# Kernel tuning notes

Hardware: AMD Instinct MI355X
Metric: run time of the kernel (lower is better)

## Reference

```python
import jax, jax.numpy as jnp
import numpy as np

N = 50000      # nodes
DIN = 512      # in_channels == in_gnn_channels == out_channels
H = 2          # num_heads
C = 512        # per-head out_channels of TransConvLayer (== in_channels)
DEMB = 256     # in_embed_features
NE = 800000    # edges (unused by transformer path)
ALPHA = 0.5
LN_EPS = 1e-5


def setup_inputs() -> dict:
    key = jax.random.key(0)
    ks = jax.random.split(key, 24)
    w = lambda k, shape, s=0.02: jax.random.normal(k, shape, jnp.float32) * s
    inp = {}
    inp["x"] = jax.random.normal(ks[0], (N, DIN), jnp.float32)
    inp["gnn_x"] = jax.random.normal(ks[1], (N, DIN), jnp.float32)
    inp["embed_x"] = jax.random.normal(ks[2], (N, DEMB), jnp.float32)
    inp["edge_index"] = jax.random.randint(ks[3], (2, NE), 0, N)
    # trans_conv input fc + layernorm
    inp["fc0_w"] = w(ks[4], (DIN, DIN)); inp["fc0_b"] = jnp.zeros((DIN,), jnp.float32)
    inp["ln0_g"] = jnp.ones((DIN,), jnp.float32); inp["ln0_b"] = jnp.zeros((DIN,), jnp.float32)
    # two TransConvLayers: Wq/Wk/Wv Linear(DIN, C*H) + post layernorm
    for i in range(2):
        base = 5 + i * 7
        inp[f"wq{i}_w"] = w(ks[base + 0], (DIN, C * H)); inp[f"wq{i}_b"] = jnp.zeros((C * H,), jnp.float32)
        inp[f"wk{i}_w"] = w(ks[base + 1], (DIN, C * H)); inp[f"wk{i}_b"] = jnp.zeros((C * H,), jnp.float32)
        inp[f"wv{i}_w"] = w(ks[base + 2], (DIN, C * H)); inp[f"wv{i}_b"] = jnp.zeros((C * H,), jnp.float32)
        inp[f"ln{i+1}_g"] = jnp.ones((DIN,), jnp.float32); inp[f"ln{i+1}_b"] = jnp.zeros((DIN,), jnp.float32)
    # SGFormer output projections: W_r (no bias), fc
    inp["wr_w"] = w(ks[20], (DIN, DIN))
    inp["fc_w"] = w(ks[21], (DIN, DIN)); inp["fc_b"] = jnp.zeros((DIN,), jnp.float32)
    return inp


def _layernorm(h, g, b):
    mu = jnp.mean(h, axis=-1, keepdims=True)
    var = jnp.mean(jnp.square(h - mu), axis=-1, keepdims=True)
    return (h - mu) * jax.lax.rsqrt(var + LN_EPS) * g + b


def _full_attention_conv(qs, ks, vs):
    # qs, ks, vs: [N, H, C]; global (Frobenius) L2 normalization, as in torch.norm(x, p=2)
    qs = qs / jnp.linalg.norm(qs)
    ks = ks / jnp.linalg.norm(ks)
    n = qs.shape[0]
    kvs = jnp.einsum('lhm,lhd->hmd', ks, vs)                   # [H, C, C]
    attn_num = jnp.einsum('nhm,hmd->nhd', qs, kvs) + n * vs    # [N, H, C]
    ks_sum = jnp.sum(ks, axis=0)                               # [H, C]
    norm = jnp.einsum('nhm,hm->nh', qs, ks_sum)[..., None] + n  # [N, H, 1]
    return attn_num / norm


def _trans_layer(h, wq_w, wq_b, wk_w, wk_b, wv_w, wv_b):
    q = (h @ wq_w + wq_b).reshape(-1, H, C)
    k = (h @ wk_w + wk_b).reshape(-1, H, C)
    v = (h @ wv_w + wv_b).reshape(-1, H, C)
    return jnp.mean(_full_attention_conv(q, k, v), axis=1)     # mean over heads -> [N, C]


def reference(x, gnn_x, embed_x, edge_index,
              fc0_w, fc0_b, ln0_g, ln0_b,
              wq0_w, wq0_b, wk0_w, wk0_b, wv0_w, wv0_b, ln1_g, ln1_b,
              wq1_w, wq1_b, wk1_w, wk1_b, wv1_w, wv1_b, ln2_g, ln2_b,
              wr_w, fc_w, fc_b):
    # use_graph=False: x, embed_x, edge_index are dead inputs (torch code computes
    # unused x_atten / scores; output depends only on gnn_x path). Eval mode: dropout off.
    h = jax.nn.relu(_layernorm(gnn_x @ fc0_w + fc0_b, ln0_g, ln0_b))
    layer_params = [
        (wq0_w, wq0_b, wk0_w, wk0_b, wv0_w, wv0_b, ln1_g, ln1_b),
        (wq1_w, wq1_b, wk1_w, wk1_b, wv1_w, wv1_b, ln2_g, ln2_b),
    ]
    for (qw, qb, kw, kb, vw, vb, lg, lb) in layer_params:
        a = _trans_layer(h, qw, qb, kw, kb, vw, vb)
        h = _layernorm(ALPHA * a + (1.0 - ALPHA) * h, lg, lb)
    return (h @ wr_w) @ fc_w + fc_b
```

## Files before the change

### kernel.cpp

```cpp
#include <hip/hip_runtime.h>

#define NN 50000
#define D 512
#define DD (512 * 512)
#define ROWS 64

typedef __attribute__((ext_vector_type(4))) float f32x4;
typedef __attribute__((ext_vector_type(8))) short bf16x8;

__device__ __forceinline__ float bf2f(unsigned short u) {
    return __uint_as_float(((unsigned int)u) << 16);
}
__device__ __forceinline__ unsigned short f2bf(float f) {
    unsigned int x = __float_as_uint(f);
    return (unsigned short)((x + 0x7fffu + ((x >> 16) & 1u)) >> 16);
}
__device__ __forceinline__ int hpos(int row, int k) {
    return (row << 9) + (((k >> 3) ^ (row & 7)) << 3) + (k & 7);
}


#define MFMA_ROW4(rf, c0, c1, c2, c3) \
    acc[rf][0] = __builtin_amdgcn_mfma_f32_16x16x32_bf16(af##rf, c0, acc[rf][0], 0, 0, 0); \
    acc[rf][1] = __builtin_amdgcn_mfma_f32_16x16x32_bf16(af##rf, c1, acc[rf][1], 0, 0, 0); \
    acc[rf][2] = __builtin_amdgcn_mfma_f32_16x16x32_bf16(af##rf, c2, acc[rf][2], 0, 0, 0); \
    acc[rf][3] = __builtin_amdgcn_mfma_f32_16x16x32_bf16(af##rf, c3, acc[rf][3], 0, 0, 0);

__global__ __launch_bounds__(512, 2)
void sg_fused(const float* __restrict__ X, const unsigned short* __restrict__ Wpack,
              const float* __restrict__ b0, const float* __restrict__ g0, const float* __restrict__ v0,
              const float* __restrict__ bm, const float* __restrict__ g1, const float* __restrict__ v1,
              const float* __restrict__ g2, const float* __restrict__ v2,
              const float* __restrict__ fcb, float* __restrict__ out)
{
    __shared__ __align__(16) unsigned short hT[ROWS * 512];
    __shared__ float Sred[8 * ROWS], Qred[8 * ROWS];
    __shared__ float MUs[ROWS], RSs[ROWS];

    const int tid = threadIdx.x;
    const int w = tid >> 6, l = tid & 63, l15 = l & 15, lhi = l >> 4;
    const int row0 = blockIdx.x * ROWS;
    const int sw = l15 & 7;
    int ccol[4];
    #pragma unroll
    for (int cf = 0; cf < 4; ++cf) ccol[cf] = w * 64 + cf * 16 + l15;

    #pragma unroll
    for (int p = 0; p < 8; ++p) {
        const int u = tid + p * 512;
        const int row = u >> 6, q = u & 63;
        bf16x8 hv = {};
        if (row0 + row < NN) {
            const f32x4* gp = reinterpret_cast<const f32x4*>(
                X + (size_t)(row0 + row) * D + q * 8);
            const f32x4 f0 = __builtin_nontemporal_load(gp);
            const f32x4 f1 = __builtin_nontemporal_load(gp + 1);
            hv[0] = (short)f2bf(f0[0]); hv[1] = (short)f2bf(f0[1]);
            hv[2] = (short)f2bf(f0[2]); hv[3] = (short)f2bf(f0[3]);
            hv[4] = (short)f2bf(f1[0]); hv[5] = (short)f2bf(f1[1]);
            hv[6] = (short)f2bf(f1[2]); hv[7] = (short)f2bf(f1[3]);
        }
        *(bf16x8*)&hT[(row << 9) + ((q ^ (row & 7)) << 3)] = hv;
    }
    __syncthreads();

    auto gemm = [&](const unsigned short* __restrict__ Wp, f32x4 (&acc)[4][4]) {
        const unsigned short* bp = Wp + (size_t)w * 32768 + (size_t)l * 8;
        bf16x8 pa0 = *(const bf16x8*)(bp);
        bf16x8 pa1 = *(const bf16x8*)(bp + 512);
        bf16x8 pa2 = *(const bf16x8*)(bp + 1024);
        bf16x8 pa3 = *(const bf16x8*)(bp + 1536);
        bf16x8 pb0 = *(const bf16x8*)(bp + 2048);
        bf16x8 pb1 = *(const bf16x8*)(bp + 2560);
        bf16x8 pb2 = *(const bf16x8*)(bp + 3072);
        bf16x8 pb3 = *(const bf16x8*)(bp + 3584);
        for (int s = 0; s < 16; s += 2) {
            {
                const int su = ((s * 4 + lhi) ^ sw) << 3;
                const bf16x8 af0 = *(const bf16x8*)&hT[((0 * 16 + l15) << 9) + su];
                const bf16x8 af1 = *(const bf16x8*)&hT[((1 * 16 + l15) << 9) + su];
                const bf16x8 af2 = *(const bf16x8*)&hT[((2 * 16 + l15) << 9) + su];
                const bf16x8 af3 = *(const bf16x8*)&hT[((3 * 16 + l15) << 9) + su];
                __builtin_amdgcn_s_setprio(1);
                MFMA_ROW4(0, pa0, pa1, pa2, pa3)
                MFMA_ROW4(1, pa0, pa1, pa2, pa3)
                MFMA_ROW4(2, pa0, pa1, pa2, pa3)
                MFMA_ROW4(3, pa0, pa1, pa2, pa3)
                __builtin_amdgcn_s_setprio(0);
                if (s + 2 < 16) {
                    const unsigned short* np = bp + (s + 2) * 2048;
                    pa0 = *(const bf16x8*)(np);
                    pa1 = *(const bf16x8*)(np + 512);
                    pa2 = *(const bf16x8*)(np + 1024);
                    pa3 = *(const bf16x8*)(np + 1536);
                }
            }
            {
                const int su = (((s + 1) * 4 + lhi) ^ sw) << 3;
                const bf16x8 af0 = *(const bf16x8*)&hT[((0 * 16 + l15) << 9) + su];
                const bf16x8 af1 = *(const bf16x8*)&hT[((1 * 16 + l15) << 9) + su];
                const bf16x8 af2 = *(const bf16x8*)&hT[((2 * 16 + l15) << 9) + su];
                const bf16x8 af3 = *(const bf16x8*)&hT[((3 * 16 + l15) << 9) + su];
                __builtin_amdgcn_s_setprio(1);
                MFMA_ROW4(0, pb0, pb1, pb2, pb3)
                MFMA_ROW4(1, pb0, pb1, pb2, pb3)
                MFMA_ROW4(2, pb0, pb1, pb2, pb3)
                MFMA_ROW4(3, pb0, pb1, pb2, pb3)
                __builtin_amdgcn_s_setprio(0);
                if (s + 3 < 16) {
                    const unsigned short* np = bp + (s + 3) * 2048;
                    pb0 = *(const bf16x8*)(np);
                    pb1 = *(const bf16x8*)(np + 512);
                    pb2 = *(const bf16x8*)(np + 1024);
                    pb3 = *(const bf16x8*)(np + 1536);
                }
            }
        }
    };

    auto lnwr = [&](f32x4 (&acc)[4][4], const float* bias, const float* g, const float* bv,
                    float eps, bool relu, bool resid) {
        float bia[4];
        #pragma unroll
        for (int cf = 0; cf < 4; ++cf) bia[cf] = bias[ccol[cf]];
        #pragma unroll
        for (int rf = 0; rf < 4; ++rf)
            #pragma unroll
            for (int reg = 0; reg < 4; ++reg) {
                const int rowl = rf * 16 + lhi * 4 + reg;
                float s = 0.f, q2 = 0.f;
                #pragma unroll
                for (int cf = 0; cf < 4; ++cf) {
                    float z = acc[rf][cf][reg] + bia[cf];
                    if (resid) z += bf2f(hT[hpos(rowl, ccol[cf])]);
                    acc[rf][cf][reg] = z;
                    s += z; q2 += z * z;
                }
                #pragma unroll
                for (int m = 1; m < 16; m <<= 1) {
                    s += __shfl_xor(s, m, 64);
                    q2 += __shfl_xor(q2, m, 64);
                }
                if (l15 == 0) { Sred[w * ROWS + rowl] = s; Qred[w * ROWS + rowl] = q2; }
            }
        __syncthreads();
        if (tid < ROWS) {
            float s = 0.f, q2 = 0.f;
            #pragma unroll
            for (int ww = 0; ww < 8; ++ww) { s += Sred[ww * ROWS + tid]; q2 += Qred[ww * ROWS + tid]; }
            const float mu = s * (1.f / 512.f);
            MUs[tid] = mu;
            RSs[tid] = rsqrtf(q2 * (1.f / 512.f) - mu * mu + eps);
        }
        __syncthreads();
        float gg[4], bb[4];
        #pragma unroll
        for (int cf = 0; cf < 4; ++cf) { gg[cf] = g[ccol[cf]]; bb[cf] = bv[ccol[cf]]; }
        #pragma unroll
        for (int rf = 0; rf < 4; ++rf)
            #pragma unroll
            for (int reg = 0; reg < 4; ++reg) {
                const int rowl = rf * 16 + lhi * 4 + reg;
                const float mu = MUs[rowl], rs = RSs[rowl];
                #pragma unroll
                for (int cf = 0; cf < 4; ++cf) {
                    float y = (acc[rf][cf][reg] - mu) * rs * gg[cf] + bb[cf];
                    if (relu) y = fmaxf(y, 0.f);
                    hT[hpos(rowl, ccol[cf])] = f2bf(y);
                }
            }
        __syncthreads();
    };

    { f32x4 acc[4][4] = {}; gemm(Wpack,          acc); lnwr(acc, b0,     g0, v0, 1e-5f, true,  false); }
    { f32x4 acc[4][4] = {}; gemm(Wpack + DD,     acc); lnwr(acc, bm,     g1, v1, 4e-5f, false, true);  }
    { f32x4 acc[4][4] = {}; gemm(Wpack + 2 * DD, acc); lnwr(acc, bm + D, g2, v2, 4e-5f, false, true);  }
    {
        f32x4 acc[4][4] = {};
        gemm(Wpack + 3 * DD, acc);
        float bia[4];
        #pragma unroll
        for (int cf = 0; cf < 4; ++cf) bia[cf] = fcb[ccol[cf]];
        #pragma unroll
        for (int rf = 0; rf < 4; ++rf)
            #pragma unroll
            for (int reg = 0; reg < 4; ++reg) {
                const int r = row0 + rf * 16 + lhi * 4 + reg;
                if (r < NN) {
                    #pragma unroll
                    for (int cf = 0; cf < 4; ++cf)
                        __builtin_nontemporal_store(acc[rf][cf][reg] + bia[cf],
                                                    &out[(size_t)r * D + ccol[cf]]);
                }
            }
    }
}


template<int FOLD>
__global__ __launch_bounds__(256)
void pack_w(const float* __restrict__ src, unsigned short* __restrict__ dst)
{
    const int t = blockIdx.x * 256 + threadIdx.x;
    const int lane = t & 63, cf = (t >> 6) & 3, kc = (t >> 8) & 15, w = t >> 12;
    const int col = w * 64 + cf * 16 + (lane & 15);
    const int k0 = kc * 32 + (lane >> 4) * 8;
    bf16x8 o;
    #pragma unroll
    for (int e = 0; e < 8; ++e) {
        float v;
        if (FOLD) v = 0.5f * (src[(size_t)(k0 + e) * 1024 + col] +
                              src[(size_t)(k0 + e) * 1024 + 512 + col]);
        else      v = src[(size_t)(k0 + e) * 512 + col];
        o[e] = (short)f2bf(v);
    }
    *(bf16x8*)(dst + (size_t)t * 8) = o;
}

__global__ __launch_bounds__(256)
void fold_bias(const float* __restrict__ bv0, const float* __restrict__ bv1,
               float* __restrict__ bm)
{
    const int d = blockIdx.x * 256 + threadIdx.x;
    if (d < 512) {
        bm[d]       = 0.5f * (bv0[d] + bv0[512 + d]);
        bm[512 + d] = 0.5f * (bv1[d] + bv1[512 + d]);
    }
}

#define FMA16(acc, a4, w4) \
    acc[0][0] += a4.x*w4.x; acc[0][1] += a4.x*w4.y; acc[0][2] += a4.x*w4.z; acc[0][3] += a4.x*w4.w; \
    acc[1][0] += a4.y*w4.x; acc[1][1] += a4.y*w4.y; acc[1][2] += a4.y*w4.z; acc[1][3] += a4.y*w4.w; \
    acc[2][0] += a4.z*w4.x; acc[2][1] += a4.z*w4.y; acc[2][2] += a4.z*w4.z; acc[2][3] += a4.z*w4.w; \
    acc[3][0] += a4.w*w4.x; acc[3][1] += a4.w*w4.y; acc[3][2] += a4.w*w4.z; acc[3][3] += a4.w*w4.w;

__global__ __launch_bounds__(256)
void gemm_f32(const float* __restrict__ A, const float* __restrict__ W,
              float* __restrict__ Cout)
{
    __shared__ __align__(16) float As[16][68];
    __shared__ __align__(16) float Ws[16][64];
    const int row0 = blockIdx.x * 64, cB = blockIdx.y * 64;
    const int tid = threadIdx.x;
    const int tx = tid & 15, ty = tid >> 4;
    const int lrow = tid >> 2, lk4 = (tid & 3) << 2;
    const int wk = tid >> 4, wc4 = (tid & 15) << 2;
    float acc[4][4] = {};
    for (int k0 = 0; k0 < 512; k0 += 16) {
        const float4 av = *reinterpret_cast<const float4*>(A + (size_t)(row0 + lrow) * 512 + k0 + lk4);
        const float4 wv = *reinterpret_cast<const float4*>(W + (size_t)(k0 + wk) * 512 + cB + wc4);
        __syncthreads();
        As[lk4 + 0][lrow] = av.x; As[lk4 + 1][lrow] = av.y;
        As[lk4 + 2][lrow] = av.z; As[lk4 + 3][lrow] = av.w;
        *reinterpret_cast<float4*>(&Ws[wk][wc4]) = wv;
        __syncthreads();
        #pragma unroll
        for (int kk = 0; kk < 16; ++kk) {
            const float4 a4 = *reinterpret_cast<const float4*>(&As[kk][ty << 2]);
            const float4 w4 = *reinterpret_cast<const float4*>(&Ws[kk][tx << 2]);
            FMA16(acc, a4, w4)
        }
    }
    #pragma unroll
    for (int i = 0; i < 4; ++i)
        *reinterpret_cast<float4*>(Cout + (size_t)(row0 + (ty << 2) + i) * 512 + cB + (tx << 2)) =
            make_float4(acc[i][0], acc[i][1], acc[i][2], acc[i][3]);
}

extern "C" void kernel_launch(void* const* d_in, const int* in_sizes, int n_in,
                              void* d_out, int out_size, void* d_ws, size_t ws_size,
                              hipStream_t stream)
{
    const float* gnn_x = (const float*)d_in[1];
    const float* fc0_w = (const float*)d_in[4];
    const float* fc0_b = (const float*)d_in[5];
    const float* ln0_g = (const float*)d_in[6];
    const float* ln0_b = (const float*)d_in[7];
    const float* wv_w[2] = {(const float*)d_in[12], (const float*)d_in[20]};
    const float* wv_b[2] = {(const float*)d_in[13], (const float*)d_in[21]};
    const float* lng[2]  = {(const float*)d_in[14], (const float*)d_in[22]};
    const float* lnb[2]  = {(const float*)d_in[15], (const float*)d_in[23]};
    const float* wr_w = (const float*)d_in[24];
    const float* fc_w = (const float*)d_in[25];
    const float* fc_b = (const float*)d_in[26];

    char* ws = (char*)d_ws;
    size_t off = 0;
    auto alloc = [&](size_t bytes) -> void* {
        void* p = ws + off;
        off += (bytes + 255) & ~(size_t)255;
        return p;
    };
    unsigned short* Wpack = (unsigned short*)alloc((size_t)4 * DD * 2);
    float*          bm    = (float*)alloc((size_t)2 * D * 4);
    float*          Wrf   = (float*)alloc((size_t)DD * 4);

    const dim3 blk256(256);

    pack_w<0><<<dim3(128), blk256, 0, stream>>>(fc0_w, Wpack);
    pack_w<1><<<dim3(128), blk256, 0, stream>>>(wv_w[0], Wpack + DD);
    pack_w<1><<<dim3(128), blk256, 0, stream>>>(wv_w[1], Wpack + 2 * DD);
    fold_bias<<<dim3(2), blk256, 0, stream>>>(wv_b[0], wv_b[1], bm);
    gemm_f32<<<dim3(8, 8), blk256, 0, stream>>>(wr_w, fc_w, Wrf);
    pack_w<0><<<dim3(128), blk256, 0, stream>>>(Wrf, Wpack + 3 * DD);

    sg_fused<<<dim3((NN + ROWS - 1) / ROWS), dim3(512), 0, stream>>>(
        gnn_x, Wpack,
        fc0_b, ln0_g, ln0_b,
        bm, lng[0], lnb[0],
        lng[1], lnb[1],
        fc_b, (float*)d_out);
}
```

Baseline: 233.4 us.

## Double block row tile to 128 with 16 waves sharing weight fragments

Raises the fused kernel's row tile from 64 to 128 rows and runs 1024-thread blocks. Waves are split into 8 column groups by 2 row groups, so each weight fragment streamed from global memory feeds twice as many rows. The LayerNorm reduction buffers and indexing are rebuilt for the 2x8 wave grid. In exchange, shared memory per block doubles to about 128KB, giving one block per CU instead of two. There are also fewer blocks in total, which can hurt tail balance and latency hiding.

```diff
diff --git a/kernel.cpp b/kernel.cpp
--- a/kernel.cpp
+++ b/kernel.cpp
@@ -3,7 +3,7 @@
 #define NN 50000
 #define D 512
 #define DD (512 * 512)
-#define ROWS 64
+#define ROWS 128
 
 typedef __attribute__((ext_vector_type(4))) float f32x4;
 typedef __attribute__((ext_vector_type(8))) short bf16x8;
@@ -26,7 +26,7 @@
     acc[rf][2] = __builtin_amdgcn_mfma_f32_16x16x32_bf16(af##rf, c2, acc[rf][2], 0, 0, 0); \
     acc[rf][3] = __builtin_amdgcn_mfma_f32_16x16x32_bf16(af##rf, c3, acc[rf][3], 0, 0, 0);
 
-__global__ __launch_bounds__(512, 2)
+__global__ __launch_bounds__(1024)
 void sg_fused(const float* __restrict__ X, const unsigned short* __restrict__ Wpack,
               const float* __restrict__ b0, const float* __restrict__ g0, const float* __restrict__ v0,
               const float* __restrict__ bm, const float* __restrict__ g1, const float* __restrict__ v1,
@@ -34,20 +34,22 @@
               const float* __restrict__ fcb, float* __restrict__ out)
 {
     __shared__ __align__(16) unsigned short hT[ROWS * 512];
-    __shared__ float Sred[8 * ROWS], Qred[8 * ROWS];
+    __shared__ float Sred[16 * 64], Qred[16 * 64];
     __shared__ float MUs[ROWS], RSs[ROWS];
 
     const int tid = threadIdx.x;
     const int w = tid >> 6, l = tid & 63, l15 = l & 15, lhi = l >> 4;
+    const int cg = w & 7, rg = w >> 3;
     const int row0 = blockIdx.x * ROWS;
     const int sw = l15 & 7;
+    const int rbase = rg * 64;
     int ccol[4];
     #pragma unroll
-    for (int cf = 0; cf < 4; ++cf) ccol[cf] = w * 64 + cf * 16 + l15;
+    for (int cf = 0; cf < 4; ++cf) ccol[cf] = cg * 64 + cf * 16 + l15;
 
     #pragma unroll
     for (int p = 0; p < 8; ++p) {
-        const int u = tid + p * 512;
+        const int u = tid + p * 1024;
         const int row = u >> 6, q = u & 63;
         bf16x8 hv = {};
         if (row0 + row < NN) {
@@ -65,7 +67,7 @@
     __syncthreads();
 
     auto gemm = [&](const unsigned short* __restrict__ Wp, f32x4 (&acc)[4][4]) {
-        const unsigned short* bp = Wp + (size_t)w * 32768 + (size_t)l * 8;
+        const unsigned short* bp = Wp + (size_t)cg * 32768 + (size_t)l * 8;
         bf16x8 pa0 = *(const bf16x8*)(bp);
         bf16x8 pa1 = *(const bf16x8*)(bp + 512);
         bf16x8 pa2 = *(const bf16x8*)(bp + 1024);
@@ -77,10 +79,10 @@
         for (int s = 0; s < 16; s += 2) {
             {
                 const int su = ((s * 4 + lhi) ^ sw) << 3;
-                const bf16x8 af0 = *(const bf16x8*)&hT[((0 * 16 + l15) << 9) + su];
-                const bf16x8 af1 = *(const bf16x8*)&hT[((1 * 16 + l15) << 9) + su];
-                const bf16x8 af2 = *(const bf16x8*)&hT[((2 * 16 + l15) << 9) + su];
-                const bf16x8 af3 = *(const bf16x8*)&hT[((3 * 16 + l15) << 9) + su];
+                const bf16x8 af0 = *(const bf16x8*)&hT[((rbase + 0 * 16 + l15) << 9) + su];
+                const bf16x8 af1 = *(const bf16x8*)&hT[((rbase + 1 * 16 + l15) << 9) + su];
+                const bf16x8 af2 = *(const bf16x8*)&hT[((rbase + 2 * 16 + l15) << 9) + su];
+                const bf16x8 af3 = *(const bf16x8*)&hT[((rbase + 3 * 16 + l15) << 9) + su];
                 __builtin_amdgcn_s_setprio(1);
                 MFMA_ROW4(0, pa0, pa1, pa2, pa3)
                 MFMA_ROW4(1, pa0, pa1, pa2, pa3)
@@ -97,10 +99,10 @@
             }
             {
                 const int su = (((s + 1) * 4 + lhi) ^ sw) << 3;
-                const bf16x8 af0 = *(const bf16x8*)&hT[((0 * 16 + l15) << 9) + su];
-                const bf16x8 af1 = *(const bf16x8*)&hT[((1 * 16 + l15) << 9) + su];
-                const bf16x8 af2 = *(const bf16x8*)&hT[((2 * 16 + l15) << 9) + su];
-                const bf16x8 af3 = *(const bf16x8*)&hT[((3 * 16 + l15) << 9) + su];
+                const bf16x8 af0 = *(const bf16x8*)&hT[((rbase + 0 * 16 + l15) << 9) + su];
+                const bf16x8 af1 = *(const bf16x8*)&hT[((rbase + 1 * 16 + l15) << 9) + su];
+                const bf16x8 af2 = *(const bf16x8*)&hT[((rbase + 2 * 16 + l15) << 9) + su];
+                const bf16x8 af3 = *(const bf16x8*)&hT[((rbase + 3 * 16 + l15) << 9) + su];
                 __builtin_amdgcn_s_setprio(1);
                 MFMA_ROW4(0, pb0, pb1, pb2, pb3)
                 MFMA_ROW4(1, pb0, pb1, pb2, pb3)
@@ -127,7 +129,8 @@
         for (int rf = 0; rf < 4; ++rf)
             #pragma unroll
             for (int reg = 0; reg < 4; ++reg) {
-                const int rowl = rf * 16 + lhi * 4 + reg;
+                const int lr = rf * 16 + lhi * 4 + reg;
+                const int rowl = rbase + lr;
                 float s = 0.f, q2 = 0.f;
                 #pragma unroll
                 for (int cf = 0; cf < 4; ++cf) {
@@ -141,13 +144,17 @@
                     s += __shfl_xor(s, m, 64);
                     q2 += __shfl_xor(q2, m, 64);
                 }
-                if (l15 == 0) { Sred[w * ROWS + rowl] = s; Qred[w * ROWS + rowl] = q2; }
+                if (l15 == 0) { Sred[w * 64 + lr] = s; Qred[w * 64 + lr] = q2; }
             }
         __syncthreads();
         if (tid < ROWS) {
+            const int rr = tid >> 6, lr = tid & 63;
             float s = 0.f, q2 = 0.f;
             #pragma unroll
-            for (int ww = 0; ww < 8; ++ww) { s += Sred[ww * ROWS + tid]; q2 += Qred[ww * ROWS + tid]; }
+            for (int cc = 0; cc < 8; ++cc) {
+                s += Sred[(rr * 8 + cc) * 64 + lr];
+                q2 += Qred[(rr * 8 + cc) * 64 + lr];
+            }
             const float mu = s * (1.f / 512.f);
             MUs[tid] = mu;
             RSs[tid] = rsqrtf(q2 * (1.f / 512.f) - mu * mu + eps);
@@ -160,7 +167,7 @@
         for (int rf = 0; rf < 4; ++rf)
             #pragma unroll
             for (int reg = 0; reg < 4; ++reg) {
-                const int rowl = rf * 16 + lhi * 4 + reg;
+                const int rowl = rbase + rf * 16 + lhi * 4 + reg;
                 const float mu = MUs[rowl], rs = RSs[rowl];
                 #pragma unroll
                 for (int cf = 0; cf < 4; ++cf) {
@@ -185,7 +192,7 @@
         for (int rf = 0; rf < 4; ++rf)
             #pragma unroll
             for (int reg = 0; reg < 4; ++reg) {
-                const int r = row0 + rf * 16 + lhi * 4 + reg;
+                const int r = row0 + rbase + rf * 16 + lhi * 4 + reg;
                 if (r < NN) {
                     #pragma unroll
                     for (int cf = 0; cf < 4; ++cf)
@@ -202,8 +209,8 @@
 void pack_w(const float* __restrict__ src, unsigned short* __restrict__ dst)
 {
     const int t = blockIdx.x * 256 + threadIdx.x;
-    const int lane = t & 63, cf = (t >> 6) & 3, kc = (t >> 8) & 15, w = t >> 12;
-    const int col = w * 64 + cf * 16 + (lane & 15);
+    const int lane = t & 63, cf = (t >> 6) & 3, kc = (t >> 8) & 15, cg = t >> 12;
+    const int col = cg * 64 + cf * 16 + (lane & 15);
     const int k0 = kc * 32 + (lane >> 4) * 8;
     bf16x8 o;
     #pragma unroll
@@ -304,7 +311,7 @@
     gemm_f32<<<dim3(8, 8), blk256, 0, stream>>>(wr_w, fc_w, Wrf);
     pack_w<0><<<dim3(128), blk256, 0, stream>>>(Wrf, Wpack + 3 * DD);
 
-    sg_fused<<<dim3((NN + ROWS - 1) / ROWS), dim3(512), 0, stream>>>(
+    sg_fused<<<dim3((NN + ROWS - 1) / ROWS), dim3(1024), 0, stream>>>(
         gnn_x, Wpack,
         fc0_b, ln0_g, ln0_b,
         bm, lng[0], lnb[0],
```

New measurement: 330.1 us. 1.41x slower.
